# Performance work log

Measured on AMD Instinct MI355X. Metric: run time of the kernel, lower is better.

## Reference

```python
import jax, jax.numpy as jnp
import numpy as np

N, E, IN, OUT, R, B = 50000, 800000, 16, 16, 90, 30


def setup_inputs() -> dict:
    key = jax.random.key(0)
    ks = jax.random.split(key, 9)
    h = jax.random.normal(ks[0], (N, IN), dtype=jnp.float32)
    he = jax.random.normal(ks[1], (E, IN), dtype=jnp.float32)
    Ws = jax.random.normal(ks[2], (OUT, IN), dtype=jnp.float32) * 0.1      # shared_weight.weight
    Wa = jax.random.normal(ks[3], (1, 3 * OUT), dtype=jnp.float32) * 0.1   # attn_fc.weight
    weight = jax.random.normal(ks[4], (B, IN, OUT), dtype=jnp.float32) * 0.1  # basis weights
    w_comp = jax.random.normal(ks[5], (R, B), dtype=jnp.float32) * 0.1        # basis coefficients
    src = jax.random.randint(ks[6], (E,), 0, N)
    dst = jax.random.randint(ks[7], (E,), 0, N)
    rel_type = jax.random.randint(ks[8], (E,), 0, R)
    return {"h": h, "he": he, "Ws": Ws, "Wa": Wa, "weight": weight,
            "w_comp": w_comp, "src": src, "dst": dst, "rel_type": rel_type}


def reference(h, he, Ws, Wa, weight, w_comp, src, dst, rel_type):
    n_nodes, in_dim = h.shape
    num_bases, _, out_dim = weight.shape
    num_rels = w_comp.shape[0]

    # Basis decomposition, replicating the original's reshape semantics exactly:
    # view [B,in,out] -> [in,B,out], matmul with w_comp [R,B] -> [in,R,out], view -> [R,in,out]
    V = weight.reshape(in_dim, num_bases, out_dim)
    W_rel = jnp.matmul(w_comp, V).reshape(num_rels, in_dim, out_dim)  # [R,in,out]

    # edge_attention: GAT-like score from concat(z_src, z_edge, z_dst)
    h_src = h[src]                      # [E,in]
    z_src = h_src @ Ws.T                # [E,out]
    z_dst = h[dst] @ Ws.T               # [E,out]
    z_e = he @ Ws.T                     # [E,out]
    e = jnp.concatenate([z_src, z_e, z_dst], axis=1) @ Wa.T  # [E,1] (no leaky_relu / no softmax in original)

    # message: per-edge relation-specific bmm, scaled by attention score
    msg = jnp.einsum('ei,eio->eo', h_src, W_rel[rel_type]) * e  # [E,out]

    # reduce: scatter-sum into destination nodes (bias=None, activation=None)
    h_out = jax.ops.segment_sum(msg, dst, num_segments=n_nodes)  # [N,out]
    return h_out
```

## Files before the change

### kernel.cpp

```cpp
#include <hip/hip_runtime.h>

#define N_NODES 50000
#define N_EDGES 800000
#define IN_DIM 16
#define OUT_DIM 16
#define N_RELS 90
#define N_BASES 30

#define CAP 24
#define LDS_STRIDE 260
#define EDGES_PER_BLK 3125

#define PREP_BLOCKS 91
#define DOTS_BLOCKS 196
#define ZERO_BLOCKS 196

__device__ __forceinline__ float4 shfl_xor4(float4 v, int m) {
    float4 r;
    r.x = __shfl_xor(v.x, m); r.y = __shfl_xor(v.y, m);
    r.z = __shfl_xor(v.z, m); r.w = __shfl_xor(v.w, m);
    return r;
}

__global__ __launch_bounds__(256) void setup_kernel(
    const float* __restrict__ Ws,
    const float* __restrict__ Wa,
    const float* __restrict__ weight,
    const float* __restrict__ w_comp,
    const float* __restrict__ h,
    float* __restrict__ Wrel,
    float* __restrict__ avec,
    float2* __restrict__ s13,
    int* __restrict__ cnt)
{
    int b = blockIdx.x;
    if (b < PREP_BLOCKS) {
        int f = b * 256 + threadIdx.x;
        if (f < N_RELS * IN_DIM * OUT_DIM) {
            int a   = f / (N_RELS * OUT_DIM);
            int rem = f % (N_RELS * OUT_DIM);
            int r   = rem / OUT_DIM;
            int o   = rem % OUT_DIM;
            float acc = 0.f;
            #pragma unroll
            for (int bb = 0; bb < N_BASES; ++bb)
                acc += w_comp[r * N_BASES + bb] * weight[a * (N_BASES * OUT_DIM) + bb * OUT_DIM + o];
            Wrel[f] = acc;
        } else if (f < N_RELS * IN_DIM * OUT_DIM + 48) {
            int g = f - N_RELS * IN_DIM * OUT_DIM;
            int k = g / IN_DIM;
            int i = g % IN_DIM;
            float acc = 0.f;
            #pragma unroll
            for (int o = 0; o < OUT_DIM; ++o)
                acc += Wa[k * OUT_DIM + o] * Ws[o * IN_DIM + i];
            avec[g] = acc;
        }
    } else if (b < PREP_BLOCKS + DOTS_BLOCKS) {
        __shared__ float la[48];
        if (threadIdx.x < 48) {
            int k = threadIdx.x / IN_DIM;
            int i = threadIdx.x % IN_DIM;
            float acc = 0.f;
            #pragma unroll
            for (int o = 0; o < OUT_DIM; ++o)
                acc += Wa[k * OUT_DIM + o] * Ws[o * IN_DIM + i];
            la[threadIdx.x] = acc;
        }
        __syncthreads();
        int n = (b - PREP_BLOCKS) * 256 + threadIdx.x;
        if (n >= N_NODES) return;
        const float4* p = (const float4*)(h + (size_t)n * IN_DIM);
        float d1 = 0.f, d3 = 0.f;
        #pragma unroll
        for (int i = 0; i < 4; ++i) {
            float4 v = p[i];
            d1 += v.x * la[4*i+0] + v.y * la[4*i+1] + v.z * la[4*i+2] + v.w * la[4*i+3];
            d3 += v.x * la[32+4*i+0] + v.y * la[32+4*i+1] + v.z * la[32+4*i+2] + v.w * la[32+4*i+3];
        }
        s13[n] = make_float2(d1, d3);
    } else {
        int n = (b - PREP_BLOCKS - DOTS_BLOCKS) * 256 + threadIdx.x;
        if (n < N_NODES) cnt[n] = 0;
    }
}

__global__ __launch_bounds__(1024) void compute_lds_kernel(
    const float* __restrict__ h,
    const float* __restrict__ he,
    const int* __restrict__ src,
    const int* __restrict__ dst,
    const int* __restrict__ rel,
    const float* __restrict__ Wrel,
    const float* __restrict__ avec,
    const float2* __restrict__ s13,
    int* __restrict__ cnt,
    float* __restrict__ bucket,
    float* __restrict__ hout)
{
    extern __shared__ float lw[];

    for (int j = threadIdx.x; j < N_RELS * 64; j += 1024) {
        int r = j >> 6;
        int w = j & 63;
        float4 v = ((const float4*)Wrel)[r * 64 + w];
        *(float4*)(lw + r * LDS_STRIDE + w * 4) = v;
    }
    __syncthreads();

    const int t = threadIdx.x;
    const int q = t & 3;
    const int grp = t >> 2;
    const int lbase = (t & 63) & ~3;
    const int ebeg = blockIdx.x * EDGES_PER_BLK;
    const int eend = ebeg + EDGES_PER_BLK;

    float4 av = *(const float4*)(avec + 16 + 4 * q);

    int e0 = ebeg + grp;
    int e1 = e0 + 256;
    int e2 = e0 + 512;

    int s0 = src[e0], d0 = dst[e0], r0 = rel[e0];
    int s1 = 0, d1 = 0, r1 = 0;
    if (e1 < eend) { s1 = src[e1]; d1 = dst[e1]; r1 = rel[e1]; }

    float4 heq0 = *(const float4*)(he + (size_t)e0 * IN_DIM + q * 4);
    float4 hq0  = *(const float4*)(h  + (size_t)s0 * IN_DIM + q * 4);
    float2 svs0 = s13[s0], svd0 = s13[d0];
    int slot0 = 0;
    if (q == 0) slot0 = atomicAdd(&cnt[d0], 1);

    for (; e0 < eend; ) {
        int s2 = 0, d2 = 0, r2 = 0;
        if (e2 < eend) { s2 = src[e2]; d2 = dst[e2]; r2 = rel[e2]; }

        float4 heq1 = {0,0,0,0}, hq1 = {0,0,0,0};
        float2 svs1 = {0,0}, svd1 = {0,0};
        int slot1 = 0;
        if (e1 < eend) {
            heq1 = *(const float4*)(he + (size_t)e1 * IN_DIM + q * 4);
            hq1  = *(const float4*)(h  + (size_t)s1 * IN_DIM + q * 4);
            svs1 = s13[s1]; svd1 = s13[d1];
            if (q == 0) slot1 = atomicAdd(&cnt[d1], 1);
        }

        int slot = __shfl(slot0, lbase);

        float pd = heq0.x * av.x + heq0.y * av.y + heq0.z * av.z + heq0.w * av.w;
        pd += __shfl_xor(pd, 1);
        pd += __shfl_xor(pd, 2);
        float score = svs0.x + svd0.y + pd;

        float4 o1 = shfl_xor4(hq0, 1);
        float4 o2 = shfl_xor4(hq0, 2);
        float4 o3 = shfl_xor4(o1, 2);
        bool q0 = (q == 0), q1 = (q == 1), q2 = (q == 2);
        float4 row0 = q0 ? hq0 : q1 ? o1 : q2 ? o2 : o3;
        float4 row1 = q0 ? o1 : q1 ? hq0 : q2 ? o3 : o2;
        float4 row2 = q0 ? o2 : q1 ? o3 : q2 ? hq0 : o1;
        float4 row3 = q0 ? o3 : q1 ? o2 : q2 ? o1 : hq0;
        float hs[16] = {row0.x,row0.y,row0.z,row0.w, row1.x,row1.y,row1.z,row1.w,
                        row2.x,row2.y,row2.z,row2.w, row3.x,row3.y,row3.z,row3.w};

        const float* wb = lw + (size_t)r0 * LDS_STRIDE + q * 4;
        float4 acc = {0.f, 0.f, 0.f, 0.f};
        #pragma unroll
        for (int i = 0; i < 16; ++i) {
            float4 w = *(const float4*)(wb + i * 16);
            float hv = hs[i];
            acc.x += hv * w.x; acc.y += hv * w.y; acc.z += hv * w.z; acc.w += hv * w.w;
        }
        acc.x *= score; acc.y *= score; acc.z *= score; acc.w *= score;

        if (slot < CAP) {
            *(float4*)(bucket + ((size_t)d0 * CAP + slot) * OUT_DIM + q * 4) = acc;
        } else {
            float* outp = hout + (size_t)d0 * OUT_DIM + q * 4;
            atomicAdd(outp + 0, acc.x);
            atomicAdd(outp + 1, acc.y);
            atomicAdd(outp + 2, acc.z);
            atomicAdd(outp + 3, acc.w);
        }

        e0 = e1; e1 = e2; e2 += 256;
        s0 = s1; d0 = d1; r0 = r1;
        s1 = s2; d1 = d2; r1 = r2;
        heq0 = heq1; hq0 = hq1; svs0 = svs1; svd0 = svd1;
        slot0 = slot1;
    }
}

__global__ __launch_bounds__(256) void reduce_bucket_kernel(
    const float* __restrict__ bucket,
    const int* __restrict__ cnt,
    float* __restrict__ hout)
{
    int tid = blockIdx.x * 256 + threadIdx.x;
    int n = tid >> 4;
    int l = tid & 15;
    int q = l & 3;
    int p = l >> 2;
    if (n >= N_NODES) return;

    int deg = cnt[n];
    int m = deg > CAP ? CAP : deg;
    const float4* bp = (const float4*)(bucket + (size_t)n * CAP * OUT_DIM) + q;
    float4 acc = {0.f, 0.f, 0.f, 0.f};
    for (int j = p; j < m; j += 4) {
        float4 v = bp[j * 4];
        acc.x += v.x; acc.y += v.y; acc.z += v.z; acc.w += v.w;
    }
    acc.x += __shfl_xor(acc.x, 4); acc.y += __shfl_xor(acc.y, 4);
    acc.z += __shfl_xor(acc.z, 4); acc.w += __shfl_xor(acc.w, 4);
    acc.x += __shfl_xor(acc.x, 8); acc.y += __shfl_xor(acc.y, 8);
    acc.z += __shfl_xor(acc.z, 8); acc.w += __shfl_xor(acc.w, 8);

    if (p == 0) {
        if (deg <= CAP) {
            *(float4*)(hout + (size_t)n * OUT_DIM + q * 4) = acc;
        } else {
            float* outp = hout + (size_t)n * OUT_DIM + q * 4;
            atomicAdd(outp + 0, acc.x);
            atomicAdd(outp + 1, acc.y);
            atomicAdd(outp + 2, acc.z);
            atomicAdd(outp + 3, acc.w);
        }
    }
}

__global__ __launch_bounds__(256) void prep_kernel(
    const float* __restrict__ Ws, const float* __restrict__ Wa,
    const float* __restrict__ weight, const float* __restrict__ w_comp,
    float* __restrict__ Wrel, float* __restrict__ avec)
{
    int f = blockIdx.x * blockDim.x + threadIdx.x;
    if (f < N_RELS * IN_DIM * OUT_DIM) {
        int a   = f / (N_RELS * OUT_DIM);
        int rem = f % (N_RELS * OUT_DIM);
        int r   = rem / OUT_DIM;
        int o   = rem % OUT_DIM;
        float acc = 0.f;
        #pragma unroll
        for (int b = 0; b < N_BASES; ++b)
            acc += w_comp[r * N_BASES + b] * weight[a * (N_BASES * OUT_DIM) + b * OUT_DIM + o];
        Wrel[f] = acc;
    } else if (f < N_RELS * IN_DIM * OUT_DIM + 48) {
        int g = f - N_RELS * IN_DIM * OUT_DIM;
        int k = g / IN_DIM;
        int i = g % IN_DIM;
        float acc = 0.f;
        #pragma unroll
        for (int o = 0; o < OUT_DIM; ++o)
            acc += Wa[k * OUT_DIM + o] * Ws[o * IN_DIM + i];
        avec[g] = acc;
    }
}

__global__ __launch_bounds__(256) void edge_atomic_kernel(
    const float* __restrict__ h,
    const float* __restrict__ he,
    const int* __restrict__ src,
    const int* __restrict__ dst,
    const int* __restrict__ rel,
    const float* __restrict__ Wrel,
    const float* __restrict__ avec,
    float* __restrict__ hout)
{
    int e = blockIdx.x * blockDim.x + threadIdx.x;
    if (e >= N_EDGES) return;
    int s = src[e], d = dst[e], r = rel[e];
    float hs[IN_DIM];
    const float4* p = (const float4*)(h + (size_t)s * IN_DIM);
    #pragma unroll
    for (int i = 0; i < 4; ++i) {
        float4 v = p[i];
        hs[4*i+0] = v.x; hs[4*i+1] = v.y; hs[4*i+2] = v.z; hs[4*i+3] = v.w;
    }
    float score = 0.f;
    #pragma unroll
    for (int i = 0; i < IN_DIM; ++i) score += hs[i] * avec[i];
    const float4* qe = (const float4*)(he + (size_t)e * IN_DIM);
    #pragma unroll
    for (int i = 0; i < 4; ++i) {
        float4 v = qe[i];
        score += v.x * avec[16+4*i] + v.y * avec[17+4*i] + v.z * avec[18+4*i] + v.w * avec[19+4*i];
    }
    const float4* pd = (const float4*)(h + (size_t)d * IN_DIM);
    #pragma unroll
    for (int i = 0; i < 4; ++i) {
        float4 v = pd[i];
        score += v.x * avec[32+4*i] + v.y * avec[33+4*i] + v.z * avec[34+4*i] + v.w * avec[35+4*i];
    }
    float acc[OUT_DIM];
    #pragma unroll
    for (int o = 0; o < OUT_DIM; ++o) acc[o] = 0.f;
    const float* W = Wrel + (size_t)r * 256;
    #pragma unroll
    for (int i = 0; i < IN_DIM; ++i) {
        float hv = hs[i];
        #pragma unroll
        for (int o = 0; o < OUT_DIM; ++o) acc[o] += hv * W[i * OUT_DIM + o];
    }
    float* outp = hout + (size_t)d * OUT_DIM;
    #pragma unroll
    for (int o = 0; o < OUT_DIM; ++o) atomicAdd(outp + o, acc[o] * score);
}

extern "C" void kernel_launch(void* const* d_in, const int* in_sizes, int n_in,
                              void* d_out, int out_size, void* d_ws, size_t ws_size,
                              hipStream_t stream) {
    const float* h      = (const float*)d_in[0];
    const float* he     = (const float*)d_in[1];
    const float* Ws     = (const float*)d_in[2];
    const float* Wa     = (const float*)d_in[3];
    const float* weight = (const float*)d_in[4];
    const float* w_comp = (const float*)d_in[5];
    const int*   src    = (const int*)d_in[6];
    const int*   dst    = (const int*)d_in[7];
    const int*   rel    = (const int*)d_in[8];
    float* hout = (float*)d_out;

    const size_t OFF_WREL   = 0;
    const size_t OFF_AVEC   = 23040;
    const size_t OFF_S13    = 23104;
    const size_t OFF_CNT    = 123104;
    const size_t OFF_BUCKET = 173104;
    const size_t NEED_BUCKET = (OFF_BUCKET + (size_t)N_NODES * CAP * OUT_DIM) * 4;

    float* wsf  = (float*)d_ws;
    float* Wrel = wsf + OFF_WREL;
    float* avec = wsf + OFF_AVEC;
    float2* s13 = (float2*)(wsf + OFF_S13);
    int* cnt    = (int*)(wsf + OFF_CNT);

    hipMemsetAsync(d_out, 0, (size_t)out_size * sizeof(float), stream);

    if (ws_size >= NEED_BUCKET) {
        float* bucket = wsf + OFF_BUCKET;

        setup_kernel<<<PREP_BLOCKS + DOTS_BLOCKS + ZERO_BLOCKS, 256, 0, stream>>>(
            Ws, Wa, weight, w_comp, h, Wrel, avec, s13, cnt);
        compute_lds_kernel<<<N_EDGES / EDGES_PER_BLK, 1024,
                             N_RELS * LDS_STRIDE * sizeof(float), stream>>>(
            h, he, src, dst, rel, Wrel, avec, s13, cnt, bucket, hout);
        reduce_bucket_kernel<<<(N_NODES * 16 + 255) / 256, 256, 0, stream>>>(
            bucket, cnt, hout);
    } else {
        int total = N_RELS * IN_DIM * OUT_DIM + 48;
        prep_kernel<<<(total + 255) / 256, 256, 0, stream>>>(Ws, Wa, weight, w_comp, Wrel, avec);
        edge_atomic_kernel<<<(N_EDGES + 255) / 256, 256, 0, stream>>>(
            h, he, src, dst, rel, Wrel, avec, hout);
    }
}
```

Measured before the change: 195.6 us.

## Batch four edges per iteration and fold output zeroing into setup kernel

The edge loop now issues index, feature and counter-atomic loads for four edges at once before computing any of them, replacing the rolling two-deep software prefetch. The aim is to keep more independent memory requests in flight per thread and hide gather latency. Separately, the output memset is removed from the bucket path and done by extra blocks in the setup kernel, saving one launch. The batching raises register pressure in a 1024-thread block, which could hurt occupancy or cause spills.

```diff
diff --git a/kernel.cpp b/kernel.cpp
--- a/kernel.cpp
+++ b/kernel.cpp
@@ -14,6 +14,7 @@
 #define PREP_BLOCKS 91
 #define DOTS_BLOCKS 196
 #define ZERO_BLOCKS 196
+#define HZ_BLOCKS 782
 
 __device__ __forceinline__ float4 shfl_xor4(float4 v, int m) {
     float4 r;
@@ -31,7 +32,8 @@
     float* __restrict__ Wrel,
     float* __restrict__ avec,
     float2* __restrict__ s13,
-    int* __restrict__ cnt)
+    int* __restrict__ cnt,
+    float* __restrict__ hout)
 {
     int b = blockIdx.x;
     if (b < PREP_BLOCKS) {
@@ -79,9 +81,15 @@
             d3 += v.x * la[32+4*i+0] + v.y * la[32+4*i+1] + v.z * la[32+4*i+2] + v.w * la[32+4*i+3];
         }
         s13[n] = make_float2(d1, d3);
-    } else {
+    } else if (b < PREP_BLOCKS + DOTS_BLOCKS + ZERO_BLOCKS) {
         int n = (b - PREP_BLOCKS - DOTS_BLOCKS) * 256 + threadIdx.x;
         if (n < N_NODES) cnt[n] = 0;
+    } else {
+        int idx = (b - PREP_BLOCKS - DOTS_BLOCKS - ZERO_BLOCKS) * 256 + threadIdx.x;
+        if (idx < N_NODES * OUT_DIM / 4) {
+            float4 z = {0.f, 0.f, 0.f, 0.f};
+            ((float4*)hout)[idx] = z;
+        }
     }
 }
 
@@ -117,77 +125,77 @@
 
     float4 av = *(const float4*)(avec + 16 + 4 * q);
 
-    int e0 = ebeg + grp;
-    int e1 = e0 + 256;
-    int e2 = e0 + 512;
-
-    int s0 = src[e0], d0 = dst[e0], r0 = rel[e0];
-    int s1 = 0, d1 = 0, r1 = 0;
-    if (e1 < eend) { s1 = src[e1]; d1 = dst[e1]; r1 = rel[e1]; }
-
-    float4 heq0 = *(const float4*)(he + (size_t)e0 * IN_DIM + q * 4);
-    float4 hq0  = *(const float4*)(h  + (size_t)s0 * IN_DIM + q * 4);
-    float2 svs0 = s13[s0], svd0 = s13[d0];
-    int slot0 = 0;
-    if (q == 0) slot0 = atomicAdd(&cnt[d0], 1);
-
-    for (; e0 < eend; ) {
-        int s2 = 0, d2 = 0, r2 = 0;
-        if (e2 < eend) { s2 = src[e2]; d2 = dst[e2]; r2 = rel[e2]; }
-
-        float4 heq1 = {0,0,0,0}, hq1 = {0,0,0,0};
-        float2 svs1 = {0,0}, svd1 = {0,0};
-        int slot1 = 0;
-        if (e1 < eend) {
-            heq1 = *(const float4*)(he + (size_t)e1 * IN_DIM + q * 4);
-            hq1  = *(const float4*)(h  + (size_t)s1 * IN_DIM + q * 4);
-            svs1 = s13[s1]; svd1 = s13[d1];
-            if (q == 0) slot1 = atomicAdd(&cnt[d1], 1);
-        }
-
-        int slot = __shfl(slot0, lbase);
-
-        float pd = heq0.x * av.x + heq0.y * av.y + heq0.z * av.z + heq0.w * av.w;
-        pd += __shfl_xor(pd, 1);
-        pd += __shfl_xor(pd, 2);
-        float score = svs0.x + svd0.y + pd;
-
-        float4 o1 = shfl_xor4(hq0, 1);
-        float4 o2 = shfl_xor4(hq0, 2);
-        float4 o3 = shfl_xor4(o1, 2);
-        bool q0 = (q == 0), q1 = (q == 1), q2 = (q == 2);
-        float4 row0 = q0 ? hq0 : q1 ? o1 : q2 ? o2 : o3;
-        float4 row1 = q0 ? o1 : q1 ? hq0 : q2 ? o3 : o2;
-        float4 row2 = q0 ? o2 : q1 ? o3 : q2 ? hq0 : o1;
-        float4 row3 = q0 ? o3 : q1 ? o2 : q2 ? o1 : hq0;
-        float hs[16] = {row0.x,row0.y,row0.z,row0.w, row1.x,row1.y,row1.z,row1.w,
-                        row2.x,row2.y,row2.z,row2.w, row3.x,row3.y,row3.z,row3.w};
-
-        const float* wb = lw + (size_t)r0 * LDS_STRIDE + q * 4;
-        float4 acc = {0.f, 0.f, 0.f, 0.f};
-        #pragma unroll
-        for (int i = 0; i < 16; ++i) {
-            float4 w = *(const float4*)(wb + i * 16);
-            float hv = hs[i];
-            acc.x += hv * w.x; acc.y += hv * w.y; acc.z += hv * w.z; acc.w += hv * w.w;
-        }
-        acc.x *= score; acc.y *= score; acc.z *= score; acc.w *= score;
-
-        if (slot < CAP) {
-            *(float4*)(bucket + ((size_t)d0 * CAP + slot) * OUT_DIM + q * 4) = acc;
-        } else {
-            float* outp = hout + (size_t)d0 * OUT_DIM + q * 4;
-            atomicAdd(outp + 0, acc.x);
-            atomicAdd(outp + 1, acc.y);
-            atomicAdd(outp + 2, acc.z);
-            atomicAdd(outp + 3, acc.w);
-        }
-
-        e0 = e1; e1 = e2; e2 += 256;
-        s0 = s1; d0 = d1; r0 = r1;
-        s1 = s2; d1 = d2; r1 = r2;
-        heq0 = heq1; hq0 = hq1; svs0 = svs1; svd0 = svd1;
-        slot0 = slot1;
+    for (int base = ebeg + grp; base < eend; base += 1024) {
+        int e[4], s[4], d[4], r[4];
+        bool val[4];
+
+        #pragma unroll
+        for (int k = 0; k < 4; ++k) {
+            e[k] = base + k * 256;
+            val[k] = (e[k] < eend);
+            int ec = val[k] ? e[k] : ebeg;
+            s[k] = src[ec]; d[k] = dst[ec]; r[k] = rel[ec];
+        }
+
+        float4 heq[4], hq[4];
+        float2 svs[4], svd[4];
+        #pragma unroll
+        for (int k = 0; k < 4; ++k) {
+            int ec = val[k] ? e[k] : ebeg;
+            heq[k] = *(const float4*)(he + (size_t)ec * IN_DIM + q * 4);
+            hq[k]  = *(const float4*)(h  + (size_t)s[k] * IN_DIM + q * 4);
+            svs[k] = s13[s[k]];
+            svd[k] = s13[d[k]];
+        }
+
+        int slot[4];
+        #pragma unroll
+        for (int k = 0; k < 4; ++k) {
+            slot[k] = 0;
+            if (q == 0 && val[k]) slot[k] = atomicAdd(&cnt[d[k]], 1);
+        }
+
+        #pragma unroll
+        for (int k = 0; k < 4; ++k) {
+            if (!val[k]) continue;
+            int sl = __shfl(slot[k], lbase);
+
+            float pd = heq[k].x * av.x + heq[k].y * av.y + heq[k].z * av.z + heq[k].w * av.w;
+            pd += __shfl_xor(pd, 1);
+            pd += __shfl_xor(pd, 2);
+            float score = svs[k].x + svd[k].y + pd;
+
+            float4 o1 = shfl_xor4(hq[k], 1);
+            float4 o2 = shfl_xor4(hq[k], 2);
+            float4 o3 = shfl_xor4(o1, 2);
+            bool q0 = (q == 0), q1 = (q == 1), q2 = (q == 2);
+            float4 row0 = q0 ? hq[k] : q1 ? o1 : q2 ? o2 : o3;
+            float4 row1 = q0 ? o1 : q1 ? hq[k] : q2 ? o3 : o2;
+            float4 row2 = q0 ? o2 : q1 ? o3 : q2 ? hq[k] : o1;
+            float4 row3 = q0 ? o3 : q1 ? o2 : q2 ? o1 : hq[k];
+            float hs[16] = {row0.x,row0.y,row0.z,row0.w, row1.x,row1.y,row1.z,row1.w,
+                            row2.x,row2.y,row2.z,row2.w, row3.x,row3.y,row3.z,row3.w};
+
+            const float* wb = lw + (size_t)r[k] * LDS_STRIDE + q * 4;
+            float4 acc = {0.f, 0.f, 0.f, 0.f};
+            #pragma unroll
+            for (int i = 0; i < 16; ++i) {
+                float4 w = *(const float4*)(wb + i * 16);
+                float hv = hs[i];
+                acc.x += hv * w.x; acc.y += hv * w.y; acc.z += hv * w.z; acc.w += hv * w.w;
+            }
+            acc.x *= score; acc.y *= score; acc.z *= score; acc.w *= score;
+
+            if (sl < CAP) {
+                *(float4*)(bucket + ((size_t)d[k] * CAP + sl) * OUT_DIM + q * 4) = acc;
+            } else {
+                float* outp = hout + (size_t)d[k] * OUT_DIM + q * 4;
+                atomicAdd(outp + 0, acc.x);
+                atomicAdd(outp + 1, acc.y);
+                atomicAdd(outp + 2, acc.z);
+                atomicAdd(outp + 3, acc.w);
+            }
+        }
     }
 }
 
@@ -334,19 +342,18 @@
     float2* s13 = (float2*)(wsf + OFF_S13);
     int* cnt    = (int*)(wsf + OFF_CNT);
 
-    hipMemsetAsync(d_out, 0, (size_t)out_size * sizeof(float), stream);
-
     if (ws_size >= NEED_BUCKET) {
         float* bucket = wsf + OFF_BUCKET;
 
-        setup_kernel<<<PREP_BLOCKS + DOTS_BLOCKS + ZERO_BLOCKS, 256, 0, stream>>>(
-            Ws, Wa, weight, w_comp, h, Wrel, avec, s13, cnt);
+        setup_kernel<<<PREP_BLOCKS + DOTS_BLOCKS + ZERO_BLOCKS + HZ_BLOCKS, 256, 0, stream>>>(
+            Ws, Wa, weight, w_comp, h, Wrel, avec, s13, cnt, hout);
         compute_lds_kernel<<<N_EDGES / EDGES_PER_BLK, 1024,
                              N_RELS * LDS_STRIDE * sizeof(float), stream>>>(
             h, he, src, dst, rel, Wrel, avec, s13, cnt, bucket, hout);
         reduce_bucket_kernel<<<(N_NODES * 16 + 255) / 256, 256, 0, stream>>>(
             bucket, cnt, hout);
     } else {
+        hipMemsetAsync(d_out, 0, (size_t)out_size * sizeof(float), stream);
         int total = N_RELS * IN_DIM * OUT_DIM + 48;
         prep_kernel<<<(total + 255) / 256, 256, 0, stream>>>(Ws, Wa, weight, w_comp, Wrel, avec);
         edge_atomic_kernel<<<(N_EDGES + 255) / 256, 256, 0, stream>>>(
```

Measured after the change: 188.6 us. 1.04x faster.
